# Kernel optimization log

Hardware: AMD Instinct MI355X
Metric: run time of the kernel (lower is better)

## Reference

```python
import jax, jax.numpy as jnp
import numpy as np

N, K, D = 32768, 8192, 512

def setup_inputs() -> dict:
    key = jax.random.key(0)
    kx, kw = jax.random.split(key)
    x = jax.random.normal(kx, (N, D), dtype=jnp.float32)
    # nn.Embedding weight init: uniform(-1/K, 1/K)
    codebook = jax.random.uniform(kw, (K, D), dtype=jnp.float32, minval=-1.0 / K, maxval=1.0 / K)
    return {"x": x, "codebook": codebook}

def reference(x, codebook):
    distances = (
        jnp.sum(x * x, axis=1, keepdims=True)
        + jnp.sum(codebook * codebook, axis=1)
        - 2.0 * jnp.einsum("nd,kd->nk", x, codebook)
    )
    encoding_indices = jnp.argmin(distances, axis=1)            # [N]
    encodings = jax.nn.one_hot(encoding_indices, K, dtype=x.dtype)  # [N, K]
    quantized = jnp.einsum("nk,kd->nd", encodings, codebook)    # [N, D]
    return quantized, encodings, encoding_indices
```

## Files before the change

kernel.cpp:

```cpp
#include <hip/hip_runtime.h>
#include <stdint.h>

#define D     512
#define BM    128
#define BN    128
#define BK    128
#define CAND  48
#define MARGIN 5e-4f
#define KDIM  8192

typedef __attribute__((ext_vector_type(4))) float f32x4;
typedef __attribute__((ext_vector_type(8))) short s16x8;
typedef unsigned long long u64;

__device__ __forceinline__ short f2bf(float f) {
  unsigned u = __float_as_uint(f);
  u = (u + 0x7FFFu + ((u >> 16) & 1u)) >> 16;
  return (short)u;
}

__device__ __forceinline__ s16x8 pack_bf8(float4 a, float4 b) {
  s16x8 v;
  v[0] = f2bf(a.x); v[1] = f2bf(a.y); v[2] = f2bf(a.z); v[3] = f2bf(a.w);
  v[4] = f2bf(b.x); v[5] = f2bf(b.y); v[6] = f2bf(b.z); v[7] = f2bf(b.w);
  return v;
}

__device__ __forceinline__ unsigned fkey(float f) {
  unsigned u = __float_as_uint(f);
  return (u >> 31) ? ~u : (u | 0x80000000u);
}
__device__ __forceinline__ float unfkey(unsigned k) {
  unsigned u = (k >> 31) ? (k & 0x7FFFFFFFu) : ~k;
  return __uint_as_float(u);
}

__global__ __launch_bounds__(256) void vq_prep(const float* __restrict__ cb,
                                               unsigned short* __restrict__ wh,
                                               float* __restrict__ b32, int K) {
  int wid  = blockIdx.x * 4 + (threadIdx.x >> 6);
  int lane = threadIdx.x & 63;
  if (wid >= K) return;
  const float* row = cb + (size_t)wid * D + lane * 8;
  float4 a = *(const float4*)row;
  float4 b = *(const float4*)(row + 4);
  float v[8] = {a.x, a.y, a.z, a.w, b.x, b.y, b.z, b.w};
  double s = 0.0;
#pragma unroll
  for (int j = 0; j < 8; ++j) { float sq = v[j] * v[j]; s += (double)sq; }
  s16x8 p = pack_bf8(a, b);
  *(s16x8*)((short*)wh + (size_t)wid * D + lane * 8) = p;
#pragma unroll
  for (int m = 1; m < 64; m <<= 1) s += __shfl_xor(s, m);
  if (lane == 0) b32[wid] = (float)s;
}

__device__ __forceinline__ void stage4(const unsigned short* __restrict__ wh,
                                       short (*wb)[BN * BK], int kt2, int c2,
                                       int w, int lane) {
#pragma unroll
  for (int i = 0; i < 4; ++i) {
    const int sb  = (w * 4 + i) * 64;
    const int s   = sb + lane;
    const int row = s >> 4;
    const int sir = s & 15;
    const int ksl = sir ^ (row & 15);
    const unsigned short* src = wh + (size_t)(kt2 * BN + row) * D + c2 * BK + ksl * 8;
    short* dst = &wb[c2][sb * 8];
    __builtin_amdgcn_global_load_lds(
        (const __attribute__((address_space(1))) unsigned int*)src,
        (__attribute__((address_space(3))) unsigned int*)dst, 16, 0, 0);
  }
}

__global__ __launch_bounds__(512, 2) void vq_main(
    const float* __restrict__ x, const float* __restrict__ cb,
    const unsigned short* __restrict__ wh, const float* __restrict__ b32g,
    float* __restrict__ out_q, float* __restrict__ out_enc, float* __restrict__ out_idx,
    int N, int K) {
  __shared__ short wb[4][BN * BK];
  __shared__ unsigned rowmin[BM];
  __shared__ unsigned rowcnt[BM];
  __shared__ unsigned candb[BM][CAND];

  const int t    = threadIdx.x;
  const int lane = t & 63;
  const int w    = t >> 6;
  const int wr   = w >> 1;
  const int wc   = w & 1;
  const int l15  = lane & 15;
  const int l16  = lane >> 4;
  const int m_base = blockIdx.x * BM;
  const int nkt  = K / BN;
  float* const enc_blk = out_enc + (size_t)m_base * K;

  if (t < BM) { rowmin[t] = 0xFFFFFFFFu; rowcnt[t] = 0u; }

  stage4(wh, wb, 0, 0, w, lane);
  stage4(wh, wb, 0, 1, w, lane);

  s16x8 afr[2][16];
#pragma unroll
  for (int mi = 0; mi < 2; ++mi) {
    const float* xr = x + (size_t)(m_base + 32 * wr + 16 * mi + l15) * D;
#pragma unroll
    for (int f = 0; f < 16; ++f) {
      const float* p = xr + (f * 4 + l16) * 8;
      float4 a = *(const float4*)p;
      float4 b = *(const float4*)(p + 4);
      afr[mi][f] = pack_bf8(a, b);
    }
  }
  __syncthreads();

  for (int kt = 0; kt < nkt; ++kt) {
    float b32v[4];
#pragma unroll
    for (int ni = 0; ni < 4; ++ni)
      b32v[ni] = b32g[kt * BN + 64 * wc + 16 * ni + l15];

    f32x4 acc[2][4];
#pragma unroll
    for (int mi = 0; mi < 2; ++mi)
#pragma unroll
      for (int ni = 0; ni < 4; ++ni) acc[mi][ni] = (f32x4){0.f, 0.f, 0.f, 0.f};

#pragma unroll
    for (int c = 0; c < 4; ++c) {
      {
        const f32x4 z4 = {0.f, 0.f, 0.f, 0.f};
        f32x4* ez = (f32x4*)(enc_blk + (size_t)kt * (BM * KDIM / 64));
        __builtin_nontemporal_store(z4, ez + (c * 2 + 0) * 512 + t);
        __builtin_nontemporal_store(z4, ez + (c * 2 + 1) * 512 + t);
      }
      const int kt2 = kt + ((c + 2) >> 2);
      if (kt2 < nkt) stage4(wh, wb, kt2, (c + 2) & 3, w, lane);

      const short* wp = &wb[c][0];
      __builtin_amdgcn_s_setprio(1);
#pragma unroll
      for (int ks = 0; ks < 4; ++ks) {
        s16x8 bfr[4];
#pragma unroll
        for (int ni = 0; ni < 4; ++ni) {
          const int row = 64 * wc + 16 * ni + l15;
          const int sl  = (ks * 4 + l16) ^ (row & 15);
          bfr[ni] = *(const s16x8*)(wp + row * BK + sl * 8);
        }
#pragma unroll
        for (int mi = 0; mi < 2; ++mi)
#pragma unroll
          for (int ni = 0; ni < 4; ++ni)
            acc[mi][ni] = __builtin_amdgcn_mfma_f32_16x16x32_bf16(
                afr[mi][c * 4 + ks], bfr[ni], acc[mi][ni], 0, 0, 0);
      }
      __builtin_amdgcn_s_setprio(0);
      if (kt2 < nkt) asm volatile("s_waitcnt vmcnt(4)" ::: "memory");
      else           asm volatile("s_waitcnt vmcnt(0)" ::: "memory");
      __builtin_amdgcn_sched_barrier(0);
      __builtin_amdgcn_s_barrier();
    }

    float tv[2][4][4];
#pragma unroll
    for (int mi = 0; mi < 2; ++mi)
#pragma unroll
      for (int ni = 0; ni < 4; ++ni)
#pragma unroll
        for (int r = 0; r < 4; ++r)
          tv[mi][ni][r] = fmaf(-2.0f, acc[mi][ni][r], b32v[ni]);

    if (kt == 0) {
#pragma unroll
      for (int mi = 0; mi < 2; ++mi)
#pragma unroll
        for (int r = 0; r < 4; ++r) {
          float m = fminf(fminf(tv[mi][0][r], tv[mi][1][r]),
                          fminf(tv[mi][2][r], tv[mi][3][r]));
          atomicMin(&rowmin[32 * wr + 16 * mi + 4 * l16 + r], fkey(m));
        }
      __syncthreads();
    }

#pragma unroll
    for (int mi = 0; mi < 2; ++mi) {
      const int rbase = 32 * wr + 16 * mi + 4 * l16;
      const uint4 ru = *(const uint4*)&rowmin[rbase];
      const unsigned rua[4] = {ru.x, ru.y, ru.z, ru.w};
#pragma unroll
      for (int r = 0; r < 4; ++r) {
        const float rm  = unfkey(rua[r]);
        const float thr = rm + MARGIN;
        const float mn  = fminf(fminf(tv[mi][0][r], tv[mi][1][r]),
                                fminf(tv[mi][2][r], tv[mi][3][r]));
        if (mn < rm) atomicMin(&rowmin[rbase + r], fkey(mn));
#pragma unroll
        for (int ni = 0; ni < 4; ++ni) {
          if (tv[mi][ni][r] <= thr) {
            unsigned p = atomicAdd(&rowcnt[rbase + r], 1u);
            if (p < CAND) candb[rbase + r][p] = (unsigned)(kt * BN + 64 * wc + 16 * ni + l15);
          }
        }
      }
    }
  }
  __syncthreads();

  for (int r = w; r < BM; r += 8) {
    const int n = m_base + r;
    const float* xr = x + (size_t)n * D + l15 * 32;
    float xv[32];
#pragma unroll
    for (int j4 = 0; j4 < 8; ++j4) {
      float4 v = *(const float4*)(xr + j4 * 4);
      xv[j4 * 4 + 0] = v.x; xv[j4 * 4 + 1] = v.y;
      xv[j4 * 4 + 2] = v.z; xv[j4 * 4 + 3] = v.w;
    }
    double s = 0.0;
#pragma unroll
    for (int j = 0; j < 32; ++j) { float sq = xv[j] * xv[j]; s += (double)sq; }
#pragma unroll
    for (int m = 1; m < 16; m <<= 1) s += __shfl_xor(s, m);
    const float Arow = (float)s;

    const unsigned cgot = rowcnt[r];
    const bool uselist = (cgot >= 1u && cgot <= (unsigned)CAND);
    const int nc = uselist ? (int)cgot : K;
    u64 best = 0xFFFFFFFFFFFFFFFFull;

    for (int i = 0; i < nc; i += 4) {
      const int ci = i + l16;
      if (ci < nc) {
        const int k = uselist ? (int)candb[r][ci] : ci;
        const float* wp = cb + (size_t)k * D + l15 * 32;
        double d = 0.0;
#pragma unroll
        for (int j4 = 0; j4 < 8; ++j4) {
          float4 v = *(const float4*)(wp + j4 * 4);
          d += (double)xv[j4 * 4 + 0] * v.x; d += (double)xv[j4 * 4 + 1] * v.y;
          d += (double)xv[j4 * 4 + 2] * v.z; d += (double)xv[j4 * 4 + 3] * v.w;
        }
#pragma unroll
        for (int m = 1; m < 16; m <<= 1) d += __shfl_xor(d, m);
        const float C32 = (float)d;
        const float T1  = Arow + b32g[k];
        const float sc  = T1 - 2.0f * C32;
        const u64 pk = ((u64)__float_as_uint(sc) << 32) | (unsigned)k;
        best = best < pk ? best : pk;
      }
    }
    {
      u64 o = __shfl_xor(best, 16); best = best < o ? best : o;
      o     = __shfl_xor(best, 32); best = best < o ? best : o;
    }
    const int kstar = (int)(best & 0xFFFFFFFFu);

    if (lane == 0) {
      out_idx[n] = (float)kstar;
      out_enc[(size_t)n * K + kstar] = 1.0f;
    }
    const float* qs = cb + (size_t)kstar * D + lane * 8;
    float4 q0 = *(const float4*)qs;
    float4 q1 = *(const float4*)(qs + 4);
    f32x4* qd = (f32x4*)(out_q + (size_t)n * D + lane * 8);
    f32x4 q0v = {q0.x, q0.y, q0.z, q0.w};
    f32x4 q1v = {q1.x, q1.y, q1.z, q1.w};
    __builtin_nontemporal_store(q0v, qd);
    __builtin_nontemporal_store(q1v, qd + 1);
  }
}

extern "C" void kernel_launch(void* const* d_in, const int* in_sizes, int n_in,
                              void* d_out, int out_size, void* d_ws, size_t ws_size,
                              hipStream_t stream) {
  const float* x  = (const float*)d_in[0];
  const float* cb = (const float*)d_in[1];
  const int N = in_sizes[0] / D;
  const int K = in_sizes[1] / D;

  unsigned short* wh = (unsigned short*)d_ws;
  float* b32 = (float*)((char*)d_ws + (size_t)K * D * sizeof(unsigned short));

  float* out     = (float*)d_out;
  float* out_q   = out;
  float* out_enc = out + (size_t)N * D;
  float* out_idx = out + (size_t)N * D + (size_t)N * K;

  vq_prep<<<(K + 3) / 4, 256, 0, stream>>>(cb, wh, b32, K);
  vq_main<<<N / BM, 512, 0, stream>>>(x, cb, wh, b32, out_q, out_enc, out_idx, N, K);
}
```

Before: 457.8 us.

## Halve row tile to 64 and switch codebook staging to double buffering

Row tile BM drops from 128 to 64, so each wave now owns one 16-row MFMA slice instead of two. That halves the A-fragment and accumulator registers and doubles the number of blocks. The LDS codebook ring shrinks from four chunks with a two-ahead prefetch to two buffers with a one-ahead prefetch, which lowers shared memory per block. In exchange, each codebook chunk loaded from global/L2 is reused by half as many rows, total codebook traffic doubles, and there is less prefetch slack to hide load latency.

```diff
diff --git a/kernel.cpp b/kernel.cpp
--- a/kernel.cpp
+++ b/kernel.cpp
@@ -2,7 +2,7 @@
 #include <stdint.h>
 
 #define D     512
-#define BM    128
+#define BM    64
 #define BN    128
 #define BK    128
 #define CAND  48
@@ -57,7 +57,7 @@
 
 __device__ __forceinline__ void stage4(const unsigned short* __restrict__ wh,
                                        short (*wb)[BN * BK], int kt2, int c2,
-                                       int w, int lane) {
+                                       int rb, int w, int lane) {
 #pragma unroll
   for (int i = 0; i < 4; ++i) {
     const int sb  = (w * 4 + i) * 64;
@@ -66,7 +66,7 @@
     const int sir = s & 15;
     const int ksl = sir ^ (row & 15);
     const unsigned short* src = wh + (size_t)(kt2 * BN + row) * D + c2 * BK + ksl * 8;
-    short* dst = &wb[c2][sb * 8];
+    short* dst = &wb[rb][sb * 8];
     __builtin_amdgcn_global_load_lds(
         (const __attribute__((address_space(1))) unsigned int*)src,
         (__attribute__((address_space(3))) unsigned int*)dst, 16, 0, 0);
@@ -78,7 +78,7 @@
     const unsigned short* __restrict__ wh, const float* __restrict__ b32g,
     float* __restrict__ out_q, float* __restrict__ out_enc, float* __restrict__ out_idx,
     int N, int K) {
-  __shared__ short wb[4][BN * BK];
+  __shared__ short wb[2][BN * BK];
   __shared__ unsigned rowmin[BM];
   __shared__ unsigned rowcnt[BM];
   __shared__ unsigned candb[BM][CAND];
@@ -96,19 +96,17 @@
 
   if (t < BM) { rowmin[t] = 0xFFFFFFFFu; rowcnt[t] = 0u; }
 
-  stage4(wh, wb, 0, 0, w, lane);
-  stage4(wh, wb, 0, 1, w, lane);
-
-  s16x8 afr[2][16];
-#pragma unroll
-  for (int mi = 0; mi < 2; ++mi) {
-    const float* xr = x + (size_t)(m_base + 32 * wr + 16 * mi + l15) * D;
+  stage4(wh, wb, 0, 0, 0, w, lane);
+
+  s16x8 afr[16];
+  {
+    const float* xr = x + (size_t)(m_base + 16 * wr + l15) * D;
 #pragma unroll
     for (int f = 0; f < 16; ++f) {
       const float* p = xr + (f * 4 + l16) * 8;
       float4 a = *(const float4*)p;
       float4 b = *(const float4*)(p + 4);
-      afr[mi][f] = pack_bf8(a, b);
+      afr[f] = pack_bf8(a, b);
     }
   }
   __syncthreads();
@@ -119,24 +117,22 @@
     for (int ni = 0; ni < 4; ++ni)
       b32v[ni] = b32g[kt * BN + 64 * wc + 16 * ni + l15];
 
-    f32x4 acc[2][4];
-#pragma unroll
-    for (int mi = 0; mi < 2; ++mi)
-#pragma unroll
-      for (int ni = 0; ni < 4; ++ni) acc[mi][ni] = (f32x4){0.f, 0.f, 0.f, 0.f};
+    f32x4 acc[4];
+#pragma unroll
+    for (int ni = 0; ni < 4; ++ni) acc[ni] = (f32x4){0.f, 0.f, 0.f, 0.f};
 
 #pragma unroll
     for (int c = 0; c < 4; ++c) {
+      const int g = kt * 4 + c;
+      const int kt2 = kt + ((c + 1) >> 2);
+      if (kt2 < nkt) stage4(wh, wb, kt2, (c + 1) & 3, (g + 1) & 1, w, lane);
       {
         const f32x4 z4 = {0.f, 0.f, 0.f, 0.f};
         f32x4* ez = (f32x4*)(enc_blk + (size_t)kt * (BM * KDIM / 64));
-        __builtin_nontemporal_store(z4, ez + (c * 2 + 0) * 512 + t);
-        __builtin_nontemporal_store(z4, ez + (c * 2 + 1) * 512 + t);
-      }
-      const int kt2 = kt + ((c + 2) >> 2);
-      if (kt2 < nkt) stage4(wh, wb, kt2, (c + 2) & 3, w, lane);
-
-      const short* wp = &wb[c][0];
+        __builtin_nontemporal_store(z4, ez + c * 512 + t);
+      }
+
+      const short* wp = &wb[g & 1][0];
       __builtin_amdgcn_s_setprio(1);
 #pragma unroll
       for (int ks = 0; ks < 4; ++ks) {
@@ -148,55 +144,46 @@
           bfr[ni] = *(const s16x8*)(wp + row * BK + sl * 8);
         }
 #pragma unroll
-        for (int mi = 0; mi < 2; ++mi)
-#pragma unroll
-          for (int ni = 0; ni < 4; ++ni)
-            acc[mi][ni] = __builtin_amdgcn_mfma_f32_16x16x32_bf16(
-                afr[mi][c * 4 + ks], bfr[ni], acc[mi][ni], 0, 0, 0);
+        for (int ni = 0; ni < 4; ++ni)
+          acc[ni] = __builtin_amdgcn_mfma_f32_16x16x32_bf16(
+              afr[c * 4 + ks], bfr[ni], acc[ni], 0, 0, 0);
       }
       __builtin_amdgcn_s_setprio(0);
-      if (kt2 < nkt) asm volatile("s_waitcnt vmcnt(4)" ::: "memory");
+      if (kt2 < nkt) asm volatile("s_waitcnt vmcnt(1)" ::: "memory");
       else           asm volatile("s_waitcnt vmcnt(0)" ::: "memory");
       __builtin_amdgcn_sched_barrier(0);
       __builtin_amdgcn_s_barrier();
     }
 
-    float tv[2][4][4];
-#pragma unroll
-    for (int mi = 0; mi < 2; ++mi)
-#pragma unroll
-      for (int ni = 0; ni < 4; ++ni)
-#pragma unroll
-        for (int r = 0; r < 4; ++r)
-          tv[mi][ni][r] = fmaf(-2.0f, acc[mi][ni][r], b32v[ni]);
+    float tv[4][4];
+#pragma unroll
+    for (int ni = 0; ni < 4; ++ni)
+#pragma unroll
+      for (int r = 0; r < 4; ++r)
+        tv[ni][r] = fmaf(-2.0f, acc[ni][r], b32v[ni]);
 
     if (kt == 0) {
 #pragma unroll
-      for (int mi = 0; mi < 2; ++mi)
-#pragma unroll
-        for (int r = 0; r < 4; ++r) {
-          float m = fminf(fminf(tv[mi][0][r], tv[mi][1][r]),
-                          fminf(tv[mi][2][r], tv[mi][3][r]));
-          atomicMin(&rowmin[32 * wr + 16 * mi + 4 * l16 + r], fkey(m));
-        }
+      for (int r = 0; r < 4; ++r) {
+        float m = fminf(fminf(tv[0][r], tv[1][r]), fminf(tv[2][r], tv[3][r]));
+        atomicMin(&rowmin[16 * wr + 4 * l16 + r], fkey(m));
+      }
       __syncthreads();
     }
 
-#pragma unroll
-    for (int mi = 0; mi < 2; ++mi) {
-      const int rbase = 32 * wr + 16 * mi + 4 * l16;
+    {
+      const int rbase = 16 * wr + 4 * l16;
       const uint4 ru = *(const uint4*)&rowmin[rbase];
       const unsigned rua[4] = {ru.x, ru.y, ru.z, ru.w};
 #pragma unroll
       for (int r = 0; r < 4; ++r) {
         const float rm  = unfkey(rua[r]);
         const float thr = rm + MARGIN;
-        const float mn  = fminf(fminf(tv[mi][0][r], tv[mi][1][r]),
-                                fminf(tv[mi][2][r], tv[mi][3][r]));
+        const float mn  = fminf(fminf(tv[0][r], tv[1][r]), fminf(tv[2][r], tv[3][r]));
         if (mn < rm) atomicMin(&rowmin[rbase + r], fkey(mn));
 #pragma unroll
         for (int ni = 0; ni < 4; ++ni) {
-          if (tv[mi][ni][r] <= thr) {
+          if (tv[ni][r] <= thr) {
             unsigned p = atomicAdd(&rowcnt[rbase + r], 1u);
             if (p < CAND) candb[rbase + r][p] = (unsigned)(kt * BN + 64 * wc + 16 * ni + l15);
           }
```

Measured after the change: 641.2 us. 1.4x slower.
